# Kernel optimization log

Measured on AMD Instinct MI355X. Metric: run time of the kernel, lower is better.

The kernel has to match this reference:

```python
import jax, jax.numpy as jnp
import numpy as np

D_MODEL = 1024
NUM_HEADS = 16
D_K = D_MODEL // NUM_HEADS


def setup_inputs() -> dict:
    key = jax.random.key(0)
    ks = jax.random.split(key, 11)
    B, S = 2, 2048
    s = 1.0 / np.sqrt(D_MODEL)
    return {
        "query": jax.random.normal(ks[0], (B, S, D_MODEL), jnp.float32),
        "key": jax.random.normal(ks[1], (B, S, D_MODEL), jnp.float32),
        "value": jax.random.normal(ks[2], (B, S, D_MODEL), jnp.float32),
        "Wq": jax.random.normal(ks[3], (D_MODEL, D_MODEL), jnp.float32) * s,
        "bq": jnp.zeros((D_MODEL,), jnp.float32),
        "Wk": jax.random.normal(ks[4], (D_MODEL, D_MODEL), jnp.float32) * s,
        "bk": jnp.zeros((D_MODEL,), jnp.float32),
        "Wv": jax.random.normal(ks[5], (D_MODEL, D_MODEL), jnp.float32) * s,
        "bv": jnp.zeros((D_MODEL,), jnp.float32),
        "Wo": jax.random.normal(ks[6], (D_MODEL, D_MODEL), jnp.float32) * s,
        "bo": jnp.zeros((D_MODEL,), jnp.float32),
    }


def _split_heads(x):
    # [B, S, D] -> [B, H, S, d_k]
    B, S, _ = x.shape
    return x.reshape(B, S, NUM_HEADS, D_K).transpose(0, 2, 1, 3)


def reference(query, key, value, Wq, bq, Wk, bk, Wv, bv, Wo, bo):
    B, S, _ = query.shape
    q = _split_heads(query @ Wq + bq)   # [B, H, S, d_k]
    k = _split_heads(key @ Wk + bk)
    v = _split_heads(value @ Wv + bv)
    scores = jnp.einsum("bhqd,bhkd->bhqk", q, k) / jnp.sqrt(jnp.float32(D_K))
    attention_weights = jax.nn.softmax(scores, axis=-1)  # [B, H, S, S]
    context = jnp.einsum("bhqk,bhkd->bhqd", attention_weights, v)
    context = context.transpose(0, 2, 1, 3).reshape(B, S, D_MODEL)
    output = context @ Wo + bo
    return (output, attention_weights)
```

## Files before the change

### kernel.cpp

```cpp
#include <hip/hip_runtime.h>
#include <hip/hip_bf16.h>


#define SEQ   2048
#define DMODEL 1024
#define NH    16
#define DKH   64

typedef __attribute__((ext_vector_type(8))) short  short8;
typedef __attribute__((ext_vector_type(4))) float  floatx4;

__device__ __forceinline__ short f2bf(float f) {
    __hip_bfloat16 h = __float2bfloat16(f);
    return *reinterpret_cast<short*>(&h);
}

__global__ void conv_f32_bf16(const float* __restrict__ src, short* __restrict__ dst, int n4) {
    int i = blockIdx.x * blockDim.x + threadIdx.x;
    if (i < n4) {
        float4 v = reinterpret_cast<const float4*>(src)[i];
        short4 o;
        o.x = f2bf(v.x); o.y = f2bf(v.y); o.z = f2bf(v.z); o.w = f2bf(v.w);
        reinterpret_cast<short4*>(dst)[i] = o;
    }
}

__global__ void conv_wt(const float* __restrict__ W, short* __restrict__ Wt) {
    int t = blockIdx.x * blockDim.x + threadIdx.x;
    int k = t >> 10, n = t & 1023;
    Wt[n * 1024 + k] = f2bf(W[t]);
}

__global__ __launch_bounds__(256, 4) void gemm_bf16(
    const short* __restrict__ A, const short* __restrict__ Bt,
    const float* __restrict__ bias, void* __restrict__ dst, int mode)
{
    __shared__ __align__(16) short As[128 * 40];
    __shared__ __align__(16) short Bs[128 * 40];
    int tid = threadIdx.x;
    int wave = tid >> 6, lane = tid & 63, quad = lane >> 4, l15 = lane & 15;
    int wy = wave >> 1, wx = wave & 1;
    int bm = blockIdx.y, bn = blockIdx.x;

    floatx4 acc[4][4];
    for (int i = 0; i < 4; i++) for (int j = 0; j < 4; j++) acc[i][j] = (floatx4){0.f, 0.f, 0.f, 0.f};

    for (int kb = 0; kb < 32; kb++) {
        for (int c = 0; c < 2; c++) {
            int ch = tid * 2 + c;
            int row = ch >> 2, kq = (ch & 3) * 8;
            *(short8*)&As[row * 40 + kq] = *(const short8*)&A [(size_t)(bm * 128 + row) * 1024 + kb * 32 + kq];
            *(short8*)&Bs[row * 40 + kq] = *(const short8*)&Bt[(size_t)(bn * 128 + row) * 1024 + kb * 32 + kq];
        }
        __syncthreads();
        short8 ar[4], br[4];
        for (int mt = 0; mt < 4; mt++) ar[mt] = *(const short8*)&As[(wy * 64 + mt * 16 + l15) * 40 + quad * 8];
        for (int nt = 0; nt < 4; nt++) br[nt] = *(const short8*)&Bs[(wx * 64 + nt * 16 + l15) * 40 + quad * 8];
        for (int mt = 0; mt < 4; mt++)
            for (int nt = 0; nt < 4; nt++)
                acc[mt][nt] = __builtin_amdgcn_mfma_f32_16x16x32_bf16(ar[mt], br[nt], acc[mt][nt], 0, 0, 0);
        __syncthreads();
    }

    for (int mt = 0; mt < 4; mt++) {
        for (int nt = 0; nt < 4; nt++) {
            int col = bn * 128 + wx * 64 + nt * 16 + l15;
            float bb = bias[col];
            for (int r = 0; r < 4; r++) {
                int row = bm * 128 + wy * 64 + mt * 16 + quad * 4 + r;
                float v = acc[mt][nt][r] + bb;
                if (mode == 3) {
                    ((float*)dst)[(size_t)row * 1024 + col] = v;
                } else {
                    int b = row >> 11, s = row & 2047, h = col >> 6, dk = col & 63;
                    size_t idx;
                    if (mode == 0) idx = ((size_t)(b * NH + h) * SEQ + s) * DKH + dk;
                    else           idx = ((size_t)(b * NH + h) * DKH + dk) * SEQ + s;
                    ((short*)dst)[idx] = f2bf(v);
                }
            }
        }
    }
}

__global__ __launch_bounds__(256, 2) void attn(
    const short* __restrict__ Q,
    const short* __restrict__ K,
    const short* __restrict__ Vt,
    float* __restrict__ wout,
    short* __restrict__ ctx)
{
    __shared__ __align__(16) short Qs [64 * 72];
    __shared__ __align__(16) short Ks [128 * 72];
    __shared__ __align__(16) short Vts[64 * 136];
    __shared__ __align__(16) short Ps [64 * 136];
    __shared__ float partial[4][64];
    __shared__ float rowsum[64];
    __shared__ float rinv[64];

    int tid = threadIdx.x, wave = tid >> 6, lane = tid & 63, quad = lane >> 4, l15 = lane & 15;
    int qt = blockIdx.x, bh = blockIdx.y;
    int b = bh >> 4, h = bh & 15;
    const short* qb  = Q  + ((size_t)bh * SEQ + qt * 64) * DKH;
    const short* kbp = K  + (size_t)bh * SEQ * DKH;
    const short* vtb = Vt + (size_t)bh * DKH * SEQ;

    for (int c = 0; c < 2; c++) {
        int ch = tid * 2 + c; int row = ch >> 3, d = (ch & 7) * 8;
        *(short8*)&Qs[row * 72 + d] = *(const short8*)&qb[row * 64 + d];
    }
    if (tid < 64) rowsum[tid] = 0.f;

    floatx4 cacc[4];
    for (int i = 0; i < 4; i++) cacc[i] = (floatx4){0.f, 0.f, 0.f, 0.f};
    int nbase = wave * 32;

    for (int kb = 0; kb < SEQ / 128; kb++) {
        __syncthreads();
        for (int c = 0; c < 4; c++) {
            int ch = tid * 4 + c; int row = ch >> 3, d = (ch & 7) * 8;
            *(short8*)&Ks[row * 72 + d] = *(const short8*)&kbp[(size_t)(kb * 128 + row) * 64 + d];
        }
        for (int c = 0; c < 4; c++) {
            int ch = tid * 4 + c; int dd = ch >> 4, kq = (ch & 15) * 8;
            *(short8*)&Vts[dd * 136 + kq] = *(const short8*)&vtb[(size_t)dd * SEQ + kb * 128 + kq];
        }
        __syncthreads();

        floatx4 sacc[4][2];
        for (int mt = 0; mt < 4; mt++) for (int nt = 0; nt < 2; nt++) sacc[mt][nt] = (floatx4){0.f, 0.f, 0.f, 0.f};
        for (int kt = 0; kt < 2; kt++) {
            short8 ar[4], br[2];
            for (int mt = 0; mt < 4; mt++) ar[mt] = *(const short8*)&Qs[(mt * 16 + l15) * 72 + kt * 32 + quad * 8];
            for (int nt = 0; nt < 2; nt++) br[nt] = *(const short8*)&Ks[(nbase + nt * 16 + l15) * 72 + kt * 32 + quad * 8];
            for (int mt = 0; mt < 4; mt++)
                for (int nt = 0; nt < 2; nt++)
                    sacc[mt][nt] = __builtin_amdgcn_mfma_f32_16x16x32_bf16(ar[mt], br[nt], sacc[mt][nt], 0, 0, 0);
        }
        for (int mt = 0; mt < 4; mt++) {
            for (int r = 0; r < 4; r++) {
                float e0 = __expf(sacc[mt][0][r] * 0.125f);
                float e1 = __expf(sacc[mt][1][r] * 0.125f);
                int row = mt * 16 + quad * 4 + r;
                Ps[row * 136 + nbase + l15]      = f2bf(e0);
                Ps[row * 136 + nbase + 16 + l15] = f2bf(e1);
                float s = e0 + e1;
                s += __shfl_xor(s, 1, 64); s += __shfl_xor(s, 2, 64);
                s += __shfl_xor(s, 4, 64); s += __shfl_xor(s, 8, 64);
                if (l15 == 0) partial[wave][row] = s;
            }
        }
        __syncthreads();
        if (tid < 64) rowsum[tid] += partial[0][tid] + partial[1][tid] + partial[2][tid] + partial[3][tid];
        for (int kt = 0; kt < 4; kt++) {
            short8 pa = *(const short8*)&Ps[(wave * 16 + l15) * 136 + kt * 32 + quad * 8];
            for (int nt = 0; nt < 4; nt++) {
                short8 vb = *(const short8*)&Vts[(nt * 16 + l15) * 136 + kt * 32 + quad * 8];
                cacc[nt] = __builtin_amdgcn_mfma_f32_16x16x32_bf16(pa, vb, cacc[nt], 0, 0, 0);
            }
        }
    }
    __syncthreads();
    if (tid < 64) rinv[tid] = 1.f / rowsum[tid];
    __syncthreads();

    for (int nt = 0; nt < 4; nt++) {
        for (int r = 0; r < 4; r++) {
            int row = wave * 16 + quad * 4 + r;
            int qg = qt * 64 + row;
            float v = cacc[nt][r] * rinv[row];
            ctx[((size_t)(b * SEQ + qg)) * DMODEL + h * DKH + nt * 16 + l15] = f2bf(v);
        }
    }

    float* wb = wout + ((size_t)bh * SEQ + qt * 64) * SEQ;
    for (int kb = 0; kb < SEQ / 128; kb++) {
        __syncthreads();
        for (int c = 0; c < 4; c++) {
            int ch = tid * 4 + c; int row = ch >> 3, d = (ch & 7) * 8;
            *(short8*)&Ks[row * 72 + d] = *(const short8*)&kbp[(size_t)(kb * 128 + row) * 64 + d];
        }
        __syncthreads();
        floatx4 sacc[4][2];
        for (int mt = 0; mt < 4; mt++) for (int nt = 0; nt < 2; nt++) sacc[mt][nt] = (floatx4){0.f, 0.f, 0.f, 0.f};
        for (int kt = 0; kt < 2; kt++) {
            short8 ar[4], br[2];
            for (int mt = 0; mt < 4; mt++) ar[mt] = *(const short8*)&Qs[(mt * 16 + l15) * 72 + kt * 32 + quad * 8];
            for (int nt = 0; nt < 2; nt++) br[nt] = *(const short8*)&Ks[(nbase + nt * 16 + l15) * 72 + kt * 32 + quad * 8];
            for (int mt = 0; mt < 4; mt++)
                for (int nt = 0; nt < 2; nt++)
                    sacc[mt][nt] = __builtin_amdgcn_mfma_f32_16x16x32_bf16(ar[mt], br[nt], sacc[mt][nt], 0, 0, 0);
        }
        for (int mt = 0; mt < 4; mt++) {
            for (int r = 0; r < 4; r++) {
                int row = mt * 16 + quad * 4 + r;
                float ri = rinv[row];
                wb[(size_t)row * SEQ + kb * 128 + nbase + l15]      = __expf(sacc[mt][0][r] * 0.125f) * ri;
                wb[(size_t)row * SEQ + kb * 128 + nbase + 16 + l15] = __expf(sacc[mt][1][r] * 0.125f) * ri;
            }
        }
    }
}

extern "C" void kernel_launch(void* const* d_in, const int* in_sizes, int n_in,
                              void* d_out, int out_size, void* d_ws, size_t ws_size,
                              hipStream_t stream) {
    const float* query = (const float*)d_in[0];
    const float* key_  = (const float*)d_in[1];
    const float* value = (const float*)d_in[2];
    const float* Wq = (const float*)d_in[3];  const float* bq = (const float*)d_in[4];
    const float* Wk = (const float*)d_in[5];  const float* bk = (const float*)d_in[6];
    const float* Wv = (const float*)d_in[7];  const float* bv = (const float*)d_in[8];
    const float* Wo = (const float*)d_in[9];  const float* bo = (const float*)d_in[10];

    char* ws = (char*)d_ws;
    const size_t MB = 1ull << 20;
    short* xq  = (short*)(ws +  0 * MB);
    short* xk  = (short*)(ws +  8 * MB);
    short* xv  = (short*)(ws + 16 * MB);
    short* wtq = (short*)(ws + 24 * MB);
    short* wtk = (short*)(ws + 26 * MB);
    short* wtv = (short*)(ws + 28 * MB);
    short* wto = (short*)(ws + 30 * MB);
    short* qh  = (short*)(ws + 32 * MB);
    short* kh  = (short*)(ws + 40 * MB);
    short* vth = (short*)(ws + 48 * MB);
    short* ctx = (short*)(ws + 56 * MB);

    float* out0 = (float*)d_out;
    float* wout = out0 + (size_t)4194304;

    conv_f32_bf16<<<4096, 256, 0, stream>>>(query, xq, 1048576);
    conv_f32_bf16<<<4096, 256, 0, stream>>>(key_,  xk, 1048576);
    conv_f32_bf16<<<4096, 256, 0, stream>>>(value, xv, 1048576);
    conv_wt<<<4096, 256, 0, stream>>>(Wq, wtq);
    conv_wt<<<4096, 256, 0, stream>>>(Wk, wtk);
    conv_wt<<<4096, 256, 0, stream>>>(Wv, wtv);
    conv_wt<<<4096, 256, 0, stream>>>(Wo, wto);

    dim3 gg(8, 32);
    gemm_bf16<<<gg, 256, 0, stream>>>(xq, wtq, bq, qh,  0);
    gemm_bf16<<<gg, 256, 0, stream>>>(xk, wtk, bk, kh,  0);
    gemm_bf16<<<gg, 256, 0, stream>>>(xv, wtv, bv, vth, 2);

    attn<<<dim3(SEQ / 64, 32), 256, 0, stream>>>(qh, kh, vth, wout, ctx);

    gemm_bf16<<<gg, 256, 0, stream>>>(ctx, wto, bo, out0, 3);
}
```

Measured before the change: 899.3 us.

## Use direct global-to-LDS loads in GEMM, tiled weight transpose, and vectorized weight writes

The GEMM tiles shrink to 128x64, and operands are loaded with global_load_lds straight into an unpadded LDS layout, which removes the register round trip and doubles the grid. The weight transpose now goes through an LDS tile so that global reads and writes are coalesced. In attention, the row sums stay in registers and are reduced once at the end, which removes a barrier-phase reduction from every iteration. The second pass permutes the K rows so each lane writes a float2 pair of adjacent softmax weights. The unpadded LDS layout in the GEMM may cause bank conflicts, and the smaller tiles lower data reuse.

```diff
diff --git a/kernel.cpp b/kernel.cpp
--- a/kernel.cpp
+++ b/kernel.cpp
@@ -13,6 +13,12 @@
 __device__ __forceinline__ short f2bf(float f) {
     __hip_bfloat16 h = __float2bfloat16(f);
     return *reinterpret_cast<short*>(&h);
+}
+
+__device__ __forceinline__ void gload_lds16(const short* g, short* l) {
+    __builtin_amdgcn_global_load_lds(
+        (const __attribute__((address_space(1))) void*)g,
+        (__attribute__((address_space(3))) void*)l, 16, 0, 0);
 }
 
 __global__ void conv_f32_bf16(const float* __restrict__ src, short* __restrict__ dst, int n4) {
@@ -26,48 +32,67 @@
 }
 
 __global__ void conv_wt(const float* __restrict__ W, short* __restrict__ Wt) {
-    int t = blockIdx.x * blockDim.x + threadIdx.x;
-    int k = t >> 10, n = t & 1023;
-    Wt[n * 1024 + k] = f2bf(W[t]);
-}
-
-__global__ __launch_bounds__(256, 4) void gemm_bf16(
+    __shared__ short T[64 * 72];
+    int tid = threadIdx.x;
+    int bk = blockIdx.y, bn = blockIdx.x;
+    for (int i = 0; i < 4; i++) {
+        int ch = i * 256 + tid;
+        int r = ch >> 4, c4 = (ch & 15) * 4;
+        float4 v = *(const float4*)&W[(size_t)(bk * 64 + r) * 1024 + bn * 64 + c4];
+        T[(c4 + 0) * 72 + r] = f2bf(v.x);
+        T[(c4 + 1) * 72 + r] = f2bf(v.y);
+        T[(c4 + 2) * 72 + r] = f2bf(v.z);
+        T[(c4 + 3) * 72 + r] = f2bf(v.w);
+    }
+    __syncthreads();
+    for (int i = 0; i < 2; i++) {
+        int ch = i * 256 + tid;
+        int n = ch >> 3, k8 = (ch & 7) * 8;
+        *(short8*)&Wt[(size_t)(bn * 64 + n) * 1024 + bk * 64 + k8] = *(const short8*)&T[n * 72 + k8];
+    }
+}
+
+__global__ __launch_bounds__(256, 3) void gemm_bf16(
     const short* __restrict__ A, const short* __restrict__ Bt,
     const float* __restrict__ bias, void* __restrict__ dst, int mode)
 {
-    __shared__ __align__(16) short As[128 * 40];
-    __shared__ __align__(16) short Bs[128 * 40];
+    __shared__ __align__(16) short As[128 * 32];
+    __shared__ __align__(16) short Bs[64 * 32];
     int tid = threadIdx.x;
     int wave = tid >> 6, lane = tid & 63, quad = lane >> 4, l15 = lane & 15;
-    int wy = wave >> 1, wx = wave & 1;
     int bm = blockIdx.y, bn = blockIdx.x;
 
-    floatx4 acc[4][4];
-    for (int i = 0; i < 4; i++) for (int j = 0; j < 4; j++) acc[i][j] = (floatx4){0.f, 0.f, 0.f, 0.f};
+    floatx4 acc[2][4];
+    for (int i = 0; i < 2; i++) for (int j = 0; j < 4; j++) acc[i][j] = (floatx4){0.f, 0.f, 0.f, 0.f};
 
     for (int kb = 0; kb < 32; kb++) {
-        for (int c = 0; c < 2; c++) {
-            int ch = tid * 2 + c;
+        for (int r = 0; r < 2; r++) {
+            int ch = r * 256 + tid;
             int row = ch >> 2, kq = (ch & 3) * 8;
-            *(short8*)&As[row * 40 + kq] = *(const short8*)&A [(size_t)(bm * 128 + row) * 1024 + kb * 32 + kq];
-            *(short8*)&Bs[row * 40 + kq] = *(const short8*)&Bt[(size_t)(bn * 128 + row) * 1024 + kb * 32 + kq];
-        }
-        __syncthreads();
-        short8 ar[4], br[4];
-        for (int mt = 0; mt < 4; mt++) ar[mt] = *(const short8*)&As[(wy * 64 + mt * 16 + l15) * 40 + quad * 8];
-        for (int nt = 0; nt < 4; nt++) br[nt] = *(const short8*)&Bs[(wx * 64 + nt * 16 + l15) * 40 + quad * 8];
-        for (int mt = 0; mt < 4; mt++)
+            gload_lds16(&A[(size_t)(bm * 128 + row) * 1024 + kb * 32 + kq],
+                        &As[(r * 256 + wave * 64) * 8]);
+        }
+        {
+            int row = tid >> 2, kq = (tid & 3) * 8;
+            gload_lds16(&Bt[(size_t)(bn * 64 + row) * 1024 + kb * 32 + kq],
+                        &Bs[(wave * 64) * 8]);
+        }
+        __syncthreads();
+        short8 ar[2], br[4];
+        for (int mt = 0; mt < 2; mt++) ar[mt] = *(const short8*)&As[(wave * 32 + mt * 16 + l15) * 32 + quad * 8];
+        for (int nt = 0; nt < 4; nt++) br[nt] = *(const short8*)&Bs[(nt * 16 + l15) * 32 + quad * 8];
+        for (int mt = 0; mt < 2; mt++)
             for (int nt = 0; nt < 4; nt++)
                 acc[mt][nt] = __builtin_amdgcn_mfma_f32_16x16x32_bf16(ar[mt], br[nt], acc[mt][nt], 0, 0, 0);
         __syncthreads();
     }
 
-    for (int mt = 0; mt < 4; mt++) {
+    for (int mt = 0; mt < 2; mt++) {
         for (int nt = 0; nt < 4; nt++) {
-            int col = bn * 128 + wx * 64 + nt * 16 + l15;
+            int col = bn * 64 + nt * 16 + l15;
             float bb = bias[col];
             for (int r = 0; r < 4; r++) {
-                int row = bm * 128 + wy * 64 + mt * 16 + quad * 4 + r;
+                int row = bm * 128 + wave * 32 + mt * 16 + quad * 4 + r;
                 float v = acc[mt][nt][r] + bb;
                 if (mode == 3) {
                     ((float*)dst)[(size_t)row * 1024 + col] = v;
@@ -95,7 +120,6 @@
     __shared__ __align__(16) short Vts[64 * 136];
     __shared__ __align__(16) short Ps [64 * 136];
     __shared__ float partial[4][64];
-    __shared__ float rowsum[64];
     __shared__ float rinv[64];
 
     int tid = threadIdx.x, wave = tid >> 6, lane = tid & 63, quad = lane >> 4, l15 = lane & 15;
@@ -109,8 +133,9 @@
         int ch = tid * 2 + c; int row = ch >> 3, d = (ch & 7) * 8;
         *(short8*)&Qs[row * 72 + d] = *(const short8*)&qb[row * 64 + d];
     }
-    if (tid < 64) rowsum[tid] = 0.f;
-
+
+    float rs[4][4];
+    for (int i = 0; i < 4; i++) for (int r = 0; r < 4; r++) rs[i][r] = 0.f;
     floatx4 cacc[4];
     for (int i = 0; i < 4; i++) cacc[i] = (floatx4){0.f, 0.f, 0.f, 0.f};
     int nbase = wave * 32;
@@ -144,14 +169,10 @@
                 int row = mt * 16 + quad * 4 + r;
                 Ps[row * 136 + nbase + l15]      = f2bf(e0);
                 Ps[row * 136 + nbase + 16 + l15] = f2bf(e1);
-                float s = e0 + e1;
-                s += __shfl_xor(s, 1, 64); s += __shfl_xor(s, 2, 64);
-                s += __shfl_xor(s, 4, 64); s += __shfl_xor(s, 8, 64);
-                if (l15 == 0) partial[wave][row] = s;
-            }
-        }
-        __syncthreads();
-        if (tid < 64) rowsum[tid] += partial[0][tid] + partial[1][tid] + partial[2][tid] + partial[3][tid];
+                rs[mt][r] += e0 + e1;
+            }
+        }
+        __syncthreads();
         for (int kt = 0; kt < 4; kt++) {
             short8 pa = *(const short8*)&Ps[(wave * 16 + l15) * 136 + kt * 32 + quad * 8];
             for (int nt = 0; nt < 4; nt++) {
@@ -160,8 +181,17 @@
             }
         }
     }
+
+    for (int mt = 0; mt < 4; mt++) {
+        for (int r = 0; r < 4; r++) {
+            float s = rs[mt][r];
+            s += __shfl_xor(s, 1, 64); s += __shfl_xor(s, 2, 64);
+            s += __shfl_xor(s, 4, 64); s += __shfl_xor(s, 8, 64);
+            if (l15 == 0) partial[wave][mt * 16 + quad * 4 + r] = s;
+        }
+    }
     __syncthreads();
-    if (tid < 64) rinv[tid] = 1.f / rowsum[tid];
+    if (tid < 64) rinv[tid] = 1.f / (partial[0][tid] + partial[1][tid] + partial[2][tid] + partial[3][tid]);
     __syncthreads();
 
     for (int nt = 0; nt < 4; nt++) {
@@ -186,7 +216,7 @@
         for (int kt = 0; kt < 2; kt++) {
             short8 ar[4], br[2];
             for (int mt = 0; mt < 4; mt++) ar[mt] = *(const short8*)&Qs[(mt * 16 + l15) * 72 + kt * 32 + quad * 8];
-            for (int nt = 0; nt < 2; nt++) br[nt] = *(const short8*)&Ks[(nbase + nt * 16 + l15) * 72 + kt * 32 + quad * 8];
+            for (int nt = 0; nt < 2; nt++) br[nt] = *(const short8*)&Ks[(nbase + 2 * l15 + nt) * 72 + kt * 32 + quad * 8];
             for (int mt = 0; mt < 4; mt++)
                 for (int nt = 0; nt < 2; nt++)
                     sacc[mt][nt] = __builtin_amdgcn_mfma_f32_16x16x32_bf16(ar[mt], br[nt], sacc[mt][nt], 0, 0, 0);
@@ -195,8 +225,10 @@
             for (int r = 0; r < 4; r++) {
                 int row = mt * 16 + quad * 4 + r;
                 float ri = rinv[row];
-                wb[(size_t)row * SEQ + kb * 128 + nbase + l15]      = __expf(sacc[mt][0][r] * 0.125f) * ri;
-                wb[(size_t)row * SEQ + kb * 128 + nbase + 16 + l15] = __expf(sacc[mt][1][r] * 0.125f) * ri;
+                float2 w2;
+                w2.x = __expf(sacc[mt][0][r] * 0.125f) * ri;
+                w2.y = __expf(sacc[mt][1][r] * 0.125f) * ri;
+                *(float2*)&wb[(size_t)row * SEQ + kb * 128 + nbase + 2 * l15] = w2;
             }
         }
     }
@@ -233,12 +265,12 @@
     conv_f32_bf16<<<4096, 256, 0, stream>>>(query, xq, 1048576);
     conv_f32_bf16<<<4096, 256, 0, stream>>>(key_,  xk, 1048576);
     conv_f32_bf16<<<4096, 256, 0, stream>>>(value, xv, 1048576);
-    conv_wt<<<4096, 256, 0, stream>>>(Wq, wtq);
-    conv_wt<<<4096, 256, 0, stream>>>(Wk, wtk);
-    conv_wt<<<4096, 256, 0, stream>>>(Wv, wtv);
-    conv_wt<<<4096, 256, 0, stream>>>(Wo, wto);
-
-    dim3 gg(8, 32);
+    conv_wt<<<dim3(16, 16), 256, 0, stream>>>(Wq, wtq);
+    conv_wt<<<dim3(16, 16), 256, 0, stream>>>(Wk, wtk);
+    conv_wt<<<dim3(16, 16), 256, 0, stream>>>(Wv, wtv);
+    conv_wt<<<dim3(16, 16), 256, 0, stream>>>(Wo, wto);
+
+    dim3 gg(16, 32);
     gemm_bf16<<<gg, 256, 0, stream>>>(xq, wtq, bq, qh,  0);
     gemm_bf16<<<gg, 256, 0, stream>>>(xk, wtk, bk, kh,  0);
     gemm_bf16<<<gg, 256, 0, stream>>>(xv, wtv, bv, vth, 2);
```

Measured after the change: 790.8 us. -12.1%, faster.
